# Kernel tuning notes

Measured on AMD Instinct MI355X. Metric: run time of the kernel, lower is better.

The kernel has to match this reference:

```python
import jax, jax.numpy as jnp
import numpy as np

TAU = 1.0
NUM_CLASSES = 14
LOSS_WEIGHT = 1.0


def setup_inputs() -> dict:
    key = jax.random.key(0)
    k1, k2, k3 = jax.random.split(key, 3)
    preds_S = jax.random.normal(k1, (2, 14, 96, 96, 96), dtype=jnp.float32)
    preds_T = jax.random.normal(k2, (2, 14, 96, 96, 96), dtype=jnp.float32)
    gt_labels = jax.random.randint(k3, (2, 1, 96, 96, 96), 0, NUM_CLASSES, dtype=jnp.int64)
    return {"preds_S": preds_S, "preds_T": preds_T, "gt_labels": gt_labels}


def reference(preds_S, preds_T, gt_labels):
    # Faithful vectorization of the nested batch/class loops:
    # softmax/log_softmax are over the CHANNEL dim (dim=0 of the [C, n_cls]
    # gathered slice), i.e. independent per voxel. Masking by class only
    # selects which voxels contribute and the mean denominator C * n_cls.
    B, C = preds_S.shape[0], preds_S.shape[1]
    S = preds_S.reshape(B, C, -1)  # [B, C, N]
    T = preds_T.reshape(B, C, -1)
    logp = jax.nn.log_softmax(S / TAU, axis=1)
    logq = jax.nn.log_softmax(T / TAU, axis=1)
    q = jnp.exp(logq)
    # pointwise KL summed over channels (torch kl_div uses xlogy: 0*log0 = 0)
    kl_pos = jnp.sum(jnp.where(q > 0, q * (logq - logp), 0.0), axis=1)  # [B, N]

    gt = gt_labels[:, 0].reshape(B, -1)  # [B, N] int labels

    def per_batch(kl_b, g_b):
        sums = jax.ops.segment_sum(kl_b, g_b, num_segments=NUM_CLASSES)
        counts = jax.ops.segment_sum(jnp.ones_like(kl_b), g_b, num_segments=NUM_CLASSES)
        return sums, counts

    sums, counts = jax.vmap(per_batch)(kl_pos, gt)  # [B, NUM_CLASSES] each
    # F.kl_div default reduction='mean': divide by total elements C * n_cls;
    # classes with zero voxels are skipped (contribute 0).
    terms = jnp.where(counts > 0, sums / (C * jnp.maximum(counts, 1.0)), 0.0)
    # class loop starts at cls=1 (background excluded despite include_background flag)
    loss = jnp.sum(terms[:, 1:]) * (TAU ** 2)
    return LOSS_WEIGHT * loss
```

## Files before the change

### kernel.cpp

```cpp
#include <hip/hip_runtime.h>
#include <stdint.h>

#define NCLS 14
#define BATCH 2
#define NUM_BINS (BATCH * NCLS)
#define KSPREAD 64


__global__ void kd_zero(float* __restrict__ fsum, int* __restrict__ fcnt) {
    int i = blockIdx.x * blockDim.x + threadIdx.x;
    fsum[i] = 0.0f;
    fcnt[i] = 0;
}

__global__ __launch_bounds__(256) void kd_kl_part(
        const float* __restrict__ S, const float* __restrict__ T,
        const int* __restrict__ gt,
        float* __restrict__ fsum, int* __restrict__ fcnt,
        int N ) {
    __shared__ float lsum[NUM_BINS];
    __shared__ int lcnt[NUM_BINS];
    if (threadIdx.x < NUM_BINS) { lsum[threadIdx.x] = 0.0f; lcnt[threadIdx.x] = 0; }
    __syncthreads();

    const int gid = blockIdx.x * blockDim.x + threadIdx.x;
    const int v0 = gid * 4;
    const int b = (v0 >= N) ? 1 : 0;
    const int n = v0 - b * N;

    const float4* Sp = reinterpret_cast<const float4*>(S + (size_t)(b * NCLS) * N + n);
    const float4* Tp = reinterpret_cast<const float4*>(T + (size_t)(b * NCLS) * N + n);
    const int quartN = N >> 2;

    float4 sv[NCLS], tv[NCLS];
#pragma unroll
    for (int c = 0; c < NCLS; ++c) sv[c] = Sp[c * quartN];
#pragma unroll
    for (int c = 0; c < NCLS; ++c) tv[c] = Tp[c * quartN];
    int4 g = *reinterpret_cast<const int4*>(gt + v0);

    float Zs[4] = {0,0,0,0}, Zt[4] = {0,0,0,0};
    float At[4] = {0,0,0,0}, As[4] = {0,0,0,0};
#pragma unroll
    for (int c = 0; c < NCLS; ++c) {
        float s[4] = {sv[c].x, sv[c].y, sv[c].z, sv[c].w};
        float t[4] = {tv[c].x, tv[c].y, tv[c].z, tv[c].w};
#pragma unroll
        for (int v = 0; v < 4; ++v) {
            float et = __expf(t[v]);
            Zt[v] += et;
            At[v] = fmaf(et, t[v], At[v]);
            As[v] = fmaf(et, s[v], As[v]);
            Zs[v] += __expf(s[v]);
        }
    }

    int cls[4] = {g.x, g.y, g.z, g.w};
#pragma unroll
    for (int v = 0; v < 4; ++v) {
        float kl = (At[v] - As[v]) / Zt[v] - __logf(Zt[v]) + __logf(Zs[v]);
        int c = min(max(cls[v], 0), NCLS - 1);
        atomicAdd(&lsum[b * NCLS + c], kl);
        atomicAdd(&lcnt[b * NCLS + c], 1);
    }

    __syncthreads();
    if (threadIdx.x < NUM_BINS) {
        const int slot = blockIdx.x & (KSPREAD - 1);
        atomicAdd(&fsum[threadIdx.x * KSPREAD + slot], lsum[threadIdx.x]);
        atomicAdd(&fcnt[threadIdx.x * KSPREAD + slot], lcnt[threadIdx.x]);
    }
}

__global__ void kd_final(const float* __restrict__ fsum,
                         const int* __restrict__ fcnt,
                         float* __restrict__ out) {
    __shared__ float terms[64];
    const int t = threadIdx.x;
    float term = 0.0f;
    if (t < NUM_BINS) {
        const float4* fp = reinterpret_cast<const float4*>(fsum + t * KSPREAD);
        const int4* cp = reinterpret_cast<const int4*>(fcnt + t * KSPREAD);
        float s = 0.0f; int n = 0;
#pragma unroll
        for (int i = 0; i < KSPREAD / 4; ++i) {
            float4 v = fp[i]; s += (v.x + v.y) + (v.z + v.w);
            int4 c = cp[i];   n += (c.x + c.y) + (c.z + c.w);
        }
        const int cls = t % NCLS;
        if (cls != 0 && n > 0) term = s / ((float)NCLS * (float)n);
    }
    terms[t] = term;
    __syncthreads();
    if (t == 0) {
        float loss = 0.0f;
#pragma unroll
        for (int i = 0; i < 64; ++i) loss += terms[i];
        out[0] = loss;
    }
}

extern "C" void kernel_launch(void* const* d_in, const int* in_sizes, int n_in,
                              void* d_out, int out_size, void* d_ws, size_t ws_size,
                              hipStream_t stream) {
    const float* S = (const float*)d_in[0];
    const float* T = (const float*)d_in[1];
    const int* gt = (const int*)d_in[2];
    float* out = (float*)d_out;

    float* fsum = (float*)d_ws;
    int* fcnt = (int*)((char*)d_ws + NUM_BINS * KSPREAD * sizeof(float));

    const int totalVox = in_sizes[2];
    const int N = totalVox / BATCH;

    const int block = 256;
    const int grid = totalVox / (block * 4);

    kd_zero<<<(NUM_BINS * KSPREAD) / 256, 256, 0, stream>>>(fsum, fcnt);
    kd_kl_part<<<grid, block, 0, stream>>>(S, T, gt, fsum, fcnt, N);
    kd_final<<<1, 64, 0, stream>>>(fsum, fcnt, out);
}
```

Baseline: 45.59 us.

## Replace global atomic reduction with per-block slot writes and single-block final reduce

Each block now writes its 28 per-bin partial sums and counts to its own workspace slot instead of doing atomic adds into spread global bins. This removes the separate zeroing kernel and the global atomic contention. The finalization becomes one 256-thread block that loops over the 28 bins, reducing across all block slots with strided loads, wave shuffles and barriers. The final kernel now serialises over bins and reads non-contiguous memory, which may cost more than the launch and atomics it replaces. The old atomic path is kept as a fallback when the workspace is too small.

```diff
diff --git a/kernel.cpp b/kernel.cpp
--- a/kernel.cpp
+++ b/kernel.cpp
@@ -4,22 +4,14 @@
 #define NCLS 14
 #define BATCH 2
 #define NUM_BINS (BATCH * NCLS)
+#define SLOT_STRIDE 32
 #define KSPREAD 64
 
 
-__global__ void kd_zero(float* __restrict__ fsum, int* __restrict__ fcnt) {
-    int i = blockIdx.x * blockDim.x + threadIdx.x;
-    fsum[i] = 0.0f;
-    fcnt[i] = 0;
-}
-
-__global__ __launch_bounds__(256) void kd_kl_part(
+__device__ __forceinline__ void kd9_compute(
         const float* __restrict__ S, const float* __restrict__ T,
-        const int* __restrict__ gt,
-        float* __restrict__ fsum, int* __restrict__ fcnt,
-        int N ) {
-    __shared__ float lsum[NUM_BINS];
-    __shared__ int lcnt[NUM_BINS];
+        const int* __restrict__ gt, int N,
+        float* lsum, int* lcnt, int* b_out) {
     if (threadIdx.x < NUM_BINS) { lsum[threadIdx.x] = 0.0f; lcnt[threadIdx.x] = 0; }
     __syncthreads();
 
@@ -27,6 +19,7 @@
     const int v0 = gid * 4;
     const int b = (v0 >= N) ? 1 : 0;
     const int n = v0 - b * N;
+    *b_out = b;
 
     const float4* Sp = reinterpret_cast<const float4*>(S + (size_t)(b * NCLS) * N + n);
     const float4* Tp = reinterpret_cast<const float4*>(T + (size_t)(b * NCLS) * N + n);
@@ -63,8 +56,69 @@
         atomicAdd(&lsum[b * NCLS + c], kl);
         atomicAdd(&lcnt[b * NCLS + c], 1);
     }
+    __syncthreads();
+}
 
-    __syncthreads();
+__global__ __launch_bounds__(256) void kd9_kl_slots(
+        const float* __restrict__ S, const float* __restrict__ T,
+        const int* __restrict__ gt,
+        float* __restrict__ fsum, int* __restrict__ fcnt, int N) {
+    __shared__ float lsum[NUM_BINS];
+    __shared__ int lcnt[NUM_BINS];
+    int b;
+    kd9_compute(S, T, gt, N, lsum, lcnt, &b);
+    if (threadIdx.x < NUM_BINS) {
+        fsum[blockIdx.x * SLOT_STRIDE + threadIdx.x] = lsum[threadIdx.x];
+        fcnt[blockIdx.x * SLOT_STRIDE + threadIdx.x] = lcnt[threadIdx.x];
+    }
+}
+
+__global__ __launch_bounds__(256) void kd9_final_slots(
+        const float* __restrict__ fsum, const int* __restrict__ fcnt,
+        float* __restrict__ out, int grid) {
+    __shared__ float wsum[4];
+    __shared__ int wcnt[4];
+    const int tid = threadIdx.x;
+    const int wave = tid >> 6, lane = tid & 63;
+    float loss = 0.0f;
+    for (int bin = 0; bin < NUM_BINS; ++bin) {
+        float s = 0.0f; int n = 0;
+        for (int i = tid; i < grid; i += 256) {
+            s += fsum[i * SLOT_STRIDE + bin];
+            n += fcnt[i * SLOT_STRIDE + bin];
+        }
+#pragma unroll
+        for (int off = 32; off >= 1; off >>= 1) {
+            s += __shfl_down(s, off);
+            n += __shfl_down(n, off);
+        }
+        if (lane == 0) { wsum[wave] = s; wcnt[wave] = n; }
+        __syncthreads();
+        if (tid == 0) {
+            float ts = wsum[0] + wsum[1] + wsum[2] + wsum[3];
+            int tn = wcnt[0] + wcnt[1] + wcnt[2] + wcnt[3];
+            int cls = bin % NCLS;
+            if (cls != 0 && tn > 0) loss += ts / ((float)NCLS * (float)tn);
+        }
+        __syncthreads();
+    }
+    if (tid == 0) out[0] = loss;
+}
+
+__global__ void kd9_zero(float* __restrict__ fsum, int* __restrict__ fcnt) {
+    int i = blockIdx.x * blockDim.x + threadIdx.x;
+    fsum[i] = 0.0f;
+    fcnt[i] = 0;
+}
+
+__global__ __launch_bounds__(256) void kd9_kl_atomic(
+        const float* __restrict__ S, const float* __restrict__ T,
+        const int* __restrict__ gt,
+        float* __restrict__ fsum, int* __restrict__ fcnt, int N) {
+    __shared__ float lsum[NUM_BINS];
+    __shared__ int lcnt[NUM_BINS];
+    int b;
+    kd9_compute(S, T, gt, N, lsum, lcnt, &b);
     if (threadIdx.x < NUM_BINS) {
         const int slot = blockIdx.x & (KSPREAD - 1);
         atomicAdd(&fsum[threadIdx.x * KSPREAD + slot], lsum[threadIdx.x]);
@@ -72,20 +126,18 @@
     }
 }
 
-__global__ void kd_final(const float* __restrict__ fsum,
-                         const int* __restrict__ fcnt,
-                         float* __restrict__ out) {
+__global__ void kd9_final_atomic(const float* __restrict__ fsum,
+                                 const int* __restrict__ fcnt,
+                                 float* __restrict__ out) {
     __shared__ float terms[64];
     const int t = threadIdx.x;
     float term = 0.0f;
     if (t < NUM_BINS) {
-        const float4* fp = reinterpret_cast<const float4*>(fsum + t * KSPREAD);
-        const int4* cp = reinterpret_cast<const int4*>(fcnt + t * KSPREAD);
         float s = 0.0f; int n = 0;
 #pragma unroll
-        for (int i = 0; i < KSPREAD / 4; ++i) {
-            float4 v = fp[i]; s += (v.x + v.y) + (v.z + v.w);
-            int4 c = cp[i];   n += (c.x + c.y) + (c.z + c.w);
+        for (int i = 0; i < KSPREAD; ++i) {
+            s += fsum[t * KSPREAD + i];
+            n += fcnt[t * KSPREAD + i];
         }
         const int cls = t % NCLS;
         if (cls != 0 && n > 0) term = s / ((float)NCLS * (float)n);
@@ -108,16 +160,23 @@
     const int* gt = (const int*)d_in[2];
     float* out = (float*)d_out;
 
-    float* fsum = (float*)d_ws;
-    int* fcnt = (int*)((char*)d_ws + NUM_BINS * KSPREAD * sizeof(float));
-
     const int totalVox = in_sizes[2];
     const int N = totalVox / BATCH;
 
     const int block = 256;
     const int grid = totalVox / (block * 4);
 
-    kd_zero<<<(NUM_BINS * KSPREAD) / 256, 256, 0, stream>>>(fsum, fcnt);
-    kd_kl_part<<<grid, block, 0, stream>>>(S, T, gt, fsum, fcnt, N);
-    kd_final<<<1, 64, 0, stream>>>(fsum, fcnt, out);
+    const size_t slot_bytes = (size_t)grid * SLOT_STRIDE * (sizeof(float) + sizeof(int));
+    if (ws_size >= slot_bytes) {
+        float* fsum = (float*)d_ws;
+        int* fcnt = (int*)((char*)d_ws + (size_t)grid * SLOT_STRIDE * sizeof(float));
+        kd9_kl_slots<<<grid, block, 0, stream>>>(S, T, gt, fsum, fcnt, N);
+        kd9_final_slots<<<1, 256, 0, stream>>>(fsum, fcnt, out, grid);
+    } else {
+        float* fsum = (float*)d_ws;
+        int* fcnt = (int*)((char*)d_ws + NUM_BINS * KSPREAD * sizeof(float));
+        kd9_zero<<<(NUM_BINS * KSPREAD) / 256, 256, 0, stream>>>(fsum, fcnt);
+        kd9_kl_atomic<<<grid, block, 0, stream>>>(S, T, gt, fsum, fcnt, N);
+        kd9_final_atomic<<<1, 64, 0, stream>>>(fsum, fcnt, out);
+    }
 }
```

New measurement: 94.88 us. +108.1%, slower.
